# Optimization experiments

Hardware: AMD Instinct MI355X
Metric: run time of the kernel (lower is better)

Reference implementation:

```python
import jax, jax.numpy as jnp
import numpy as np


def setup_inputs() -> dict:
    key = jax.random.key(0)
    B, S, V = 4, 4096, 32000
    x = jax.random.randint(key, (B, S), 0, V, dtype=jnp.int32)
    return {"x": x, "d_vocab": V}


def reference(x, d_vocab):
    # Math identical to: gather(cumsum(one_hot(x, d_vocab), axis=1), x)
    # i.e. counts[b, s] = #{t <= s : x[b, t] == x[b, s]} (inclusive running count).
    # Implemented as an O(seq) scan over per-vocab counters instead of
    # materializing the [B, S, V] one-hot cumsum.
    B, S = x.shape
    batch_idx = jnp.arange(B)

    def step(counters, xt):  # counters: [B, V], xt: [B]
        counters = counters.at[batch_idx, xt].add(1.0)
        return counters, counters[batch_idx, xt]

    init = jnp.zeros((B, d_vocab), dtype=jnp.float32)
    _, counts = jax.lax.scan(step, init, x.T)  # counts: [S, B]
    return counts.T[..., None]  # [B, S, 1] float32, matching torch gather output
```

## Files before the change

### kernel.cpp

```cpp
#include <hip/hip_runtime.h>


#define SEQ 4096
#define QT  256
#define CT  256

__global__ __launch_bounds__(256)
void zero_out_kernel(float4* __restrict__ out) {
    out[blockIdx.x * 256 + threadIdx.x] = make_float4(0.f, 0.f, 0.f, 0.f);
}

__global__ __launch_bounds__(256)
void count_partial_kernel(const int* __restrict__ x, float* __restrict__ out) {
    const int c  = blockIdx.x;
    const int qt = blockIdx.y;
    const int b  = blockIdx.z;
    if (c > qt) return;

    const int tid = threadIdx.x;
    const int* __restrict__ row = x + b * SEQ;
    const int s = qt * QT + tid;
    const int q = row[s];

    __shared__ int tile[CT];
    tile[tid] = row[c * CT + tid];
    __syncthreads();

    int cnt = 0;
    if (c < qt) {
        #pragma unroll 8
        for (int k = 0; k < CT; k += 4) {
            int4 a = *reinterpret_cast<const int4*>(&tile[k]);
            cnt += (q == a.x) + (q == a.y) + (q == a.z) + (q == a.w);
        }
    } else {
        #pragma unroll 8
        for (int k = 0; k < CT; k += 4) {
            int4 a = *reinterpret_cast<const int4*>(&tile[k]);
            cnt += (int)((k + 0 <= tid) & (q == a.x))
                 + (int)((k + 1 <= tid) & (q == a.y))
                 + (int)((k + 2 <= tid) & (q == a.z))
                 + (int)((k + 3 <= tid) & (q == a.w));
        }
    }
    atomicAdd(&out[b * SEQ + s], (float)cnt);
}

extern "C" void kernel_launch(void* const* d_in, const int* in_sizes, int n_in,
                              void* d_out, int out_size, void* d_ws, size_t ws_size,
                              hipStream_t stream) {
    const int* x = (const int*)d_in[0];
    float* out = (float*)d_out;
    const int B = in_sizes[0] / SEQ;

    zero_out_kernel<<<dim3(out_size / (4 * 256)), 256, 0, stream>>>((float4*)out);

    count_partial_kernel<<<dim3(SEQ / CT, SEQ / QT, B), 256, 0, stream>>>(x, out);
}
```

Measured before the change: 63.04 us.

## Loop over key tiles inside each block and drop zeroing and atomics

Replaces the 2D grid of (key tile, query tile) blocks with one block per query tile that loops over all earlier key tiles in shared memory, then handles the diagonal tile. This removes the separate zero-fill kernel and the float atomicAdd, writing each output directly. The cost is far less parallelism: only 16*B = 64 blocks, with heavy load imbalance (the last tile loops 15 times), plus two barriers per iteration, so the GPU may be badly underoccupied.

```diff
diff --git a/kernel.cpp b/kernel.cpp
--- a/kernel.cpp
+++ b/kernel.cpp
@@ -2,48 +2,42 @@
 
 
 #define SEQ 4096
-#define QT  256
-#define CT  256
 
 __global__ __launch_bounds__(256)
-void zero_out_kernel(float4* __restrict__ out) {
-    out[blockIdx.x * 256 + threadIdx.x] = make_float4(0.f, 0.f, 0.f, 0.f);
-}
-
-__global__ __launch_bounds__(256)
-void count_partial_kernel(const int* __restrict__ x, float* __restrict__ out) {
-    const int c  = blockIdx.x;
-    const int qt = blockIdx.y;
-    const int b  = blockIdx.z;
-    if (c > qt) return;
-
+void count_kernel(const int* __restrict__ x, float* __restrict__ out) {
+    const int qt  = blockIdx.x;
+    const int b   = blockIdx.y;
     const int tid = threadIdx.x;
     const int* __restrict__ row = x + b * SEQ;
-    const int s = qt * QT + tid;
+    const int s = (qt << 8) + tid;
     const int q = row[s];
 
-    __shared__ int tile[CT];
-    tile[tid] = row[c * CT + tid];
-    __syncthreads();
+    __shared__ int tile[256];
+    int cnt = 0;
 
-    int cnt = 0;
-    if (c < qt) {
-        #pragma unroll 8
-        for (int k = 0; k < CT; k += 4) {
+    for (int c = 0; c < qt; ++c) {
+        tile[tid] = row[(c << 8) + tid];
+        __syncthreads();
+        #pragma unroll 16
+        for (int k = 0; k < 256; k += 4) {
             int4 a = *reinterpret_cast<const int4*>(&tile[k]);
             cnt += (q == a.x) + (q == a.y) + (q == a.z) + (q == a.w);
         }
-    } else {
-        #pragma unroll 8
-        for (int k = 0; k < CT; k += 4) {
-            int4 a = *reinterpret_cast<const int4*>(&tile[k]);
-            cnt += (int)((k + 0 <= tid) & (q == a.x))
-                 + (int)((k + 1 <= tid) & (q == a.y))
-                 + (int)((k + 2 <= tid) & (q == a.z))
-                 + (int)((k + 3 <= tid) & (q == a.w));
-        }
+        __syncthreads();
     }
-    atomicAdd(&out[b * SEQ + s], (float)cnt);
+
+    tile[tid] = q;
+    __syncthreads();
+    #pragma unroll 16
+    for (int k = 0; k < 256; k += 4) {
+        int4 a = *reinterpret_cast<const int4*>(&tile[k]);
+        cnt += (int)((k + 0 <= tid) & (q == a.x))
+             + (int)((k + 1 <= tid) & (q == a.y))
+             + (int)((k + 2 <= tid) & (q == a.z))
+             + (int)((k + 3 <= tid) & (q == a.w));
+    }
+
+    out[b * SEQ + s] = (float)cnt;
 }
 
 extern "C" void kernel_launch(void* const* d_in, const int* in_sizes, int n_in,
@@ -53,7 +47,5 @@
     float* out = (float*)d_out;
     const int B = in_sizes[0] / SEQ;
 
-    zero_out_kernel<<<dim3(out_size / (4 * 256)), 256, 0, stream>>>((float4*)out);
-
-    count_partial_kernel<<<dim3(SEQ / CT, SEQ / QT, B), 256, 0, stream>>>(x, out);
+    count_kernel<<<dim3(SEQ / 256, B), 256, 0, stream>>>(x, out);
 }
```

New measurement: 84.78 us. 1.34x slower.
